# Kernel tuning notes

Measured on AMD Instinct MI355X. Metric: run time of the kernel, lower is better.

Reference implementation:

```python
import jax, jax.numpy as jnp
import numpy as np

N = 50000      # nodes
E = 800000     # edges (before self loops)
D_IN = 64      # input atom feature dim
HID = 128      # hidden_dim
HEADS = 4
C = HID // HEADS  # 32 per-head channels
ED = 12        # edge feature dim
L = 4          # num GAT layers
EPS = 1e-5


def setup_inputs() -> dict:
    key = jax.random.key(0)
    ks = jax.random.split(key, 10)
    s = 0.1
    return {
        "x": jax.random.normal(ks[0], (N, D_IN), jnp.float32),
        "edge_index": jax.random.randint(ks[1], (2, E), 0, N, dtype=jnp.int32),
        "edge_attr": jax.random.uniform(ks[2], (E, ED), jnp.float32),
        "Wp": jax.random.normal(ks[3], (D_IN, HID), jnp.float32) * s,
        "bp": jnp.zeros((HID,), jnp.float32),
        "W": jax.random.normal(ks[4], (L, HID, HID), jnp.float32) * s,
        "We": jax.random.normal(ks[5], (L, ED, HID), jnp.float32) * s,
        "att_src": jax.random.normal(ks[6], (L, HEADS, C), jnp.float32) * s,
        "att_dst": jax.random.normal(ks[7], (L, HEADS, C), jnp.float32) * s,
        "att_edge": jax.random.normal(ks[8], (L, HEADS, C), jnp.float32) * s,
        "bias": jnp.zeros((L, HID), jnp.float32),
        "gamma": jnp.ones((L, HID), jnp.float32),
        "beta": jnp.zeros((L, HID), jnp.float32),
    }


def _gat_layer(h, src, dst, ea_full, W, We, a_s, a_d, a_e, b):
    # PyG GATConv: x' = x W -> [N, heads, C]; attention uses edge features, msg = alpha * x'_src
    xp = (h @ W).reshape(N, HEADS, C)
    e_emb = (ea_full @ We).reshape(-1, HEADS, C)          # [E', heads, C]
    a_src = (xp * a_s).sum(-1)                            # [N, heads]
    a_dst = (xp * a_d).sum(-1)
    a = a_src[src] + a_dst[dst] + (e_emb * a_e).sum(-1)   # [E', heads]
    a = jax.nn.leaky_relu(a, 0.2)
    # segment softmax over destination node neighborhoods
    amax = jax.ops.segment_max(a, dst, num_segments=N)
    ex = jnp.exp(a - amax[dst])
    denom = jax.ops.segment_sum(ex, dst, num_segments=N)
    alpha = ex / denom[dst]                               # [E', heads]
    msg = alpha[:, :, None] * xp[src]                     # [E', heads, C]
    out = jax.ops.segment_sum(msg, dst, num_segments=N)   # [N, heads, C]
    return out.reshape(N, HID) + b


def reference(x, edge_index, edge_attr, Wp, bp, W, We, att_src, att_dst, att_edge, bias, gamma, beta):
    # PyG GATConv add_self_loops=True with fill_value='mean' for edge_attr
    loop = jnp.arange(N, dtype=edge_index.dtype)
    src = jnp.concatenate([edge_index[0], loop])
    dst = jnp.concatenate([edge_index[1], loop])
    ea_mean = edge_attr.mean(0)
    ea_full = jnp.concatenate([edge_attr, jnp.broadcast_to(ea_mean, (N, ED))], 0)

    h = jax.nn.relu(x @ Wp + bp)
    for i in range(L):
        h_in = h
        h = _gat_layer(h, src, dst, ea_full, W[i], We[i], att_src[i], att_dst[i], att_edge[i], bias[i])
        # BatchNorm1d (training-mode batch statistics)
        mu = h.mean(0)
        var = ((h - mu) ** 2).mean(0)
        h = gamma[i] * (h - mu) / jnp.sqrt(var + EPS) + beta[i]
        h = jax.nn.relu(h)
        if i > 0:
            h = h + h_in
    return h
```

## Files before the change

### kernel.cpp

```cpp
#include <hip/hip_runtime.h>

constexpr int N_NODES = 50000;
constexpr int N_EDGES = 800000;
constexpr int N_ETOT  = N_EDGES + N_NODES;
constexpr int HID     = 128;
constexpr int HEADS   = 4;
constexpr int ED      = 12;
constexpr int LAYERS  = 4;
constexpr float BN_EPS = 1e-5f;
constexpr int R_REP = 4;
constexpr int RN = N_NODES * R_REP;
constexpr int SB2 = (RN + 255) / 256;
constexpr int EB = (N_ETOT + 255) / 256;
constexpr int GB = (N_NODES + 63) / 64;
constexpr int WB = (LAYERS * HID * HID + 255) / 256;

typedef __attribute__((ext_vector_type(8))) short short8;
typedef __attribute__((ext_vector_type(4))) float floatx4;

__device__ inline unsigned bf16pair(float a, float b) {
    unsigned ua = __float_as_uint(a), ub = __float_as_uint(b);
    ua = (ua + 0x7FFFu + ((ua >> 16) & 1u)) >> 16;
    ub = (ub + 0x7FFFu + ((ub >> 16) & 1u)) >> 16;
    return ua | (ub << 16);
}

__launch_bounds__(256)
__global__ void pre1_kernel(const int* __restrict__ dst, int* __restrict__ hist2,
                            int* __restrict__ rank,
                            const float* __restrict__ ea, float* __restrict__ easum,
                            const float* __restrict__ W, unsigned short* __restrict__ wb,
                            const float* __restrict__ A, const float* __restrict__ B,
                            const float* __restrict__ bias, float* __restrict__ C,
                            unsigned* __restrict__ Cb) {
    __shared__ float smem[64 * 128];
    int bid = blockIdx.x, t = threadIdx.x;
    if (bid < GB) {
        constexpr int K = 64;
        const float4* B4 = (const float4*)B;
        float4* Bs4 = (float4*)smem;
#pragma unroll
        for (int i = t; i < K * 32; i += 256) Bs4[i] = B4[i];
        __syncthreads();

        int c0 = (t & 15) * 8;
        int r0 = (t >> 4) * 4;
        int rbase = bid * 64 + r0;

        float acc[4][8];
#pragma unroll
        for (int j = 0; j < 4; j++)
#pragma unroll
            for (int c = 0; c < 8; c++) acc[j][c] = 0.f;

        const float4* A4 = (const float4*)A;
        int rg[4];
#pragma unroll
        for (int j = 0; j < 4; j++) rg[j] = min(rbase + j, N_NODES - 1);

        for (int kk = 0; kk < K; kk += 4) {
            float4 av[4];
#pragma unroll
            for (int j = 0; j < 4; j++) av[j] = A4[(size_t)rg[j] * (K / 4) + (kk >> 2)];
            float a_arr[4][4];
#pragma unroll
            for (int j = 0; j < 4; j++) {
                a_arr[j][0] = av[j].x; a_arr[j][1] = av[j].y;
                a_arr[j][2] = av[j].z; a_arr[j][3] = av[j].w;
            }
#pragma unroll
            for (int jj = 0; jj < 4; jj++) {
                float4 b0 = Bs4[(kk + jj) * 32 + (c0 >> 2)];
                float4 b1 = Bs4[(kk + jj) * 32 + (c0 >> 2) + 1];
#pragma unroll
                for (int j = 0; j < 4; j++) {
                    float a = a_arr[j][jj];
                    acc[j][0] += a * b0.x; acc[j][1] += a * b0.y;
                    acc[j][2] += a * b0.z; acc[j][3] += a * b0.w;
                    acc[j][4] += a * b1.x; acc[j][5] += a * b1.y;
                    acc[j][6] += a * b1.z; acc[j][7] += a * b1.w;
                }
            }
        }

#pragma unroll
        for (int j = 0; j < 4; j++) {
            int r = rbase + j;
            if (r < N_NODES) {
                float o[8];
#pragma unroll
                for (int c = 0; c < 8; c++) o[c] = fmaxf(acc[j][c] + bias[c0 + c], 0.f);
                ((float4*)(C + (size_t)r * 128 + c0))[0] = make_float4(o[0], o[1], o[2], o[3]);
                ((float4*)(C + (size_t)r * 128 + c0 + 4))[0] = make_float4(o[4], o[5], o[6], o[7]);
                uint4 pk;
                pk.x = bf16pair(o[0], o[1]); pk.y = bf16pair(o[2], o[3]);
                pk.z = bf16pair(o[4], o[5]); pk.w = bf16pair(o[6], o[7]);
                ((uint4*)(Cb + (size_t)r * 64 + (c0 >> 1)))[0] = pk;
            }
        }
    } else if (bid < GB + EB) {
        int e = (bid - GB) * 256 + t;
        if (e < N_ETOT) {
            int d = (e < N_EDGES) ? dst[e] : (e - N_EDGES);
            rank[e] = atomicAdd(&hist2[(e & (R_REP - 1)) * N_NODES + d], 1);
        }
    } else if (bid < GB + EB + 256) {
        int b2 = bid - GB - EB;
        float* ls = smem;
        if (t < 12) ls[t] = 0.f;
        __syncthreads();
        float loc[12];
#pragma unroll
        for (int d = 0; d < 12; d++) loc[d] = 0.f;
        for (int e = b2 * 256 + t; e < N_EDGES; e += 256 * 256) {
            const float* er = ea + (size_t)e * ED;
#pragma unroll
            for (int d = 0; d < 12; d++) loc[d] += er[d];
        }
#pragma unroll
        for (int d = 0; d < 12; d++) atomicAdd(&ls[d], loc[d]);
        __syncthreads();
        if (t < 12) atomicAdd(&easum[t], ls[t]);
    } else {
        int idx = (bid - GB - EB - 256) * 256 + t;
        if (idx < LAYERS * HID * HID) {
            int l = idx >> 14;
            int k = (idx >> 7) & 127;
            int n = idx & 127;
            unsigned u = __float_as_uint(W[idx]);
            u = (u + 0x7FFFu + ((u >> 16) & 1u)) >> 16;
            int kt = k >> 5, q = (k & 31) >> 3, j = k & 7;
            int nt = n >> 4, c = n & 15;
            int lane = q * 16 + c;
            wb[(size_t)l * 16384 + ((size_t)(kt * 8 + nt) * 64 + lane) * 8 + j] =
                (unsigned short)u;
        }
    }
}

__global__ void blocksum_kernel(const int* __restrict__ hist2, int* __restrict__ bsum) {
    __shared__ int sd[256];
    int t = threadIdx.x;
    int f = blockIdx.x * 256 + t;
    int v = 0;
    if (f < RN) v = hist2[(f & (R_REP - 1)) * N_NODES + (f >> 2)];
    sd[t] = v;
    __syncthreads();
#pragma unroll
    for (int off = 128; off; off >>= 1) {
        if (t < off) sd[t] += sd[t + off];
        __syncthreads();
    }
    if (t == 0) bsum[blockIdx.x] = sd[0];
}

__launch_bounds__(256)
__global__ void pre2_kernel(const int* __restrict__ bsum, int* __restrict__ boff,
                            int* __restrict__ rowpR, const float* __restrict__ easum,
                            const float* __restrict__ We, const float* __restrict__ att_edge,
                            float* __restrict__ wea_all, float* __restrict__ aloop) {
    int t = threadIdx.x;
    if (blockIdx.x == 0) {
        __shared__ int sd[256];
        int b = 4 * t;
        int v0 = (b + 0 < SB2) ? bsum[b + 0] : 0;
        int v1 = (b + 1 < SB2) ? bsum[b + 1] : 0;
        int v2 = (b + 2 < SB2) ? bsum[b + 2] : 0;
        int v3 = (b + 3 < SB2) ? bsum[b + 3] : 0;
        int tot = v0 + v1 + v2 + v3;
        sd[t] = tot;
        __syncthreads();
#pragma unroll
        for (int off = 1; off < 256; off <<= 1) {
            int u = (t >= off) ? sd[t - off] : 0;
            __syncthreads();
            sd[t] += u;
            __syncthreads();
        }
        int excl = sd[t] - tot;
        if (b + 0 < SB2) boff[b + 0] = excl;
        if (b + 1 < SB2) boff[b + 1] = excl + v0;
        if (b + 2 < SB2) boff[b + 2] = excl + v0 + v1;
        if (b + 3 < SB2) boff[b + 3] = excl + v0 + v1 + v2;
        if (t == 255) rowpR[RN] = sd[255];
    } else {
        __shared__ float em[12];
        __shared__ float weash[LAYERS * ED * HEADS];
        if (t < 12) em[t] = easum[t] / (float)N_EDGES;
        if (t < LAYERS * ED * HEADS) {
            int l = t / (ED * HEADS);
            int r = t % (ED * HEADS);
            int d = r / HEADS;
            int h = r % HEADS;
            float sum = 0.f;
#pragma unroll
            for (int c = 0; c < 32; c++)
                sum += We[((size_t)(l * ED + d)) * HID + h * 32 + c] *
                       att_edge[(l * HEADS + h) * 32 + c];
            wea_all[t] = sum;
            weash[t] = sum;
        }
        __syncthreads();
        if (t < LAYERS * HEADS) {
            int l = t / HEADS, h = t % HEADS;
            float s = 0.f;
#pragma unroll
            for (int d = 0; d < 12; d++) s += em[d] * weash[l * ED * HEADS + d * HEADS + h];
            aloop[t] = s;
        }
    }
}

__global__ void rowp_kernel(const int* __restrict__ hist2, const int* __restrict__ boff,
                            int* __restrict__ rowpR) {
    __shared__ int sd[256];
    int t = threadIdx.x;
    int f = blockIdx.x * 256 + t;
    int v = (f < RN) ? hist2[(f & (R_REP - 1)) * N_NODES + (f >> 2)] : 0;
    sd[t] = v;
    __syncthreads();
#pragma unroll
    for (int off = 1; off < 256; off <<= 1) {
        int u = (t >= off) ? sd[t - off] : 0;
        __syncthreads();
        sd[t] += u;
        __syncthreads();
    }
    if (f < RN) rowpR[f] = sd[t] - v + boff[blockIdx.x];
}

__launch_bounds__(256)
__global__ void pre3_kernel(const unsigned short* __restrict__ hAb,
                            const unsigned short* __restrict__ wb,
                            const float* __restrict__ att_s, const float* __restrict__ att_d,
                            unsigned* __restrict__ xpb,
                            float* __restrict__ asrc, float* __restrict__ adst,
                            const int* __restrict__ src, const int* __restrict__ dst,
                            const int* __restrict__ rank, const int* __restrict__ rowpR,
                            int2* __restrict__ csr) {
    __shared__ float smem[4 * 16 * 129];
    int t = threadIdx.x;
    if (blockIdx.x >= GB) {
        int e = (blockIdx.x - GB) * 256 + t;
        if (e >= N_ETOT) return;
        int s, d;
        if (e < N_EDGES) { s = src[e]; d = dst[e]; }
        else             { s = d = e - N_EDGES; }
        int pos = rowpR[d * R_REP + (e & (R_REP - 1))] + rank[e];
        csr[pos] = make_int2(s, e);
        return;
    }
    int bid = blockIdx.x;
    float (*lds)[16][129] = (float (*)[16][129])smem;
    int w = t >> 6, lane = t & 63;
    int rbase = bid * 64 + w * 16;
    int mrow = lane & 15, quad = lane >> 4;

    floatx4 acc[8];
#pragma unroll
    for (int nt = 0; nt < 8; nt++) acc[nt] = (floatx4){0.f, 0.f, 0.f, 0.f};

    int arow = min(rbase + mrow, N_NODES - 1);
    const short8* wb8 = (const short8*)wb;
#pragma unroll
    for (int kt = 0; kt < 4; kt++) {
        short8 afrag = *(const short8*)(hAb + (size_t)arow * 128 + kt * 32 + quad * 8);
#pragma unroll
        for (int nt = 0; nt < 8; nt++) {
            short8 bfrag = wb8[(kt * 8 + nt) * 64 + lane];
            acc[nt] = __builtin_amdgcn_mfma_f32_16x16x32_bf16(afrag, bfrag, acc[nt], 0, 0, 0);
        }
    }
#pragma unroll
    for (int nt = 0; nt < 8; nt++)
#pragma unroll
        for (int rr = 0; rr < 4; rr++)
            lds[w][quad * 4 + rr][nt * 16 + mrow] = acc[nt][rr];

    int row = lane >> 2, h = lane & 3;
    int r = rbase + row;
    float vals[32];
    float ps = 0.f, pd = 0.f;
#pragma unroll
    for (int c = 0; c < 32; c++) {
        float v = lds[w][row][h * 32 + c];
        vals[c] = v;
        ps += v * att_s[h * 32 + c];
        pd += v * att_d[h * 32 + c];
    }
    if (r < N_NODES) {
        unsigned* dstp = xpb + (size_t)r * 64 + h * 16;
#pragma unroll
        for (int qq = 0; qq < 4; qq++) {
            uint4 o;
            o.x = bf16pair(vals[qq * 8 + 0], vals[qq * 8 + 1]);
            o.y = bf16pair(vals[qq * 8 + 2], vals[qq * 8 + 3]);
            o.z = bf16pair(vals[qq * 8 + 4], vals[qq * 8 + 5]);
            o.w = bf16pair(vals[qq * 8 + 6], vals[qq * 8 + 7]);
            ((uint4*)dstp)[qq] = o;
        }
        asrc[r * 4 + h] = ps;
        adst[r * 4 + h] = pd;
    }
}

__launch_bounds__(256)
__global__ void pre4_kernel(const int2* __restrict__ csr, const float* __restrict__ ea,
                            const float* __restrict__ wea_all, const float* __restrict__ aloop,
                            uint2* __restrict__ aecsr) {
    __shared__ float wsh[LAYERS * ED * HEADS];
    __shared__ float lsh[LAYERS * HEADS];
    int t = threadIdx.x;
    if (t < LAYERS * ED * HEADS) wsh[t] = wea_all[t];
    if (t < LAYERS * HEADS) lsh[t] = aloop[t];
    __syncthreads();
    int i = blockIdx.x * 256 + t;
    if (i >= N_ETOT) return;
    int e = csr[i].y;
    float a[LAYERS][4];
    if (e < N_EDGES) {
        float er[12];
        const float* ep = ea + (size_t)e * ED;
#pragma unroll
        for (int d = 0; d < 12; d++) er[d] = ep[d];
#pragma unroll
        for (int l = 0; l < LAYERS; l++)
#pragma unroll
            for (int h = 0; h < 4; h++) {
                float s = 0.f;
#pragma unroll
                for (int d = 0; d < 12; d++) s += er[d] * wsh[l * 48 + d * 4 + h];
                a[l][h] = s;
            }
    } else {
#pragma unroll
        for (int l = 0; l < LAYERS; l++)
#pragma unroll
            for (int h = 0; h < 4; h++) a[l][h] = lsh[l * 4 + h];
    }
#pragma unroll
    for (int l = 0; l < LAYERS; l++)
        aecsr[(size_t)l * N_ETOT + i] =
            make_uint2(bf16pair(a[l][0], a[l][1]), bf16pair(a[l][2], a[l][3]));
}

template <int ADD>
__launch_bounds__(256)
__global__ void gemm_fused_kernel(const float* __restrict__ outb,
                                  const float* __restrict__ bnsum,
                                  const float* __restrict__ bnsum2,
                                  const float* __restrict__ gamma,
                                  const float* __restrict__ beta,
                                  float* __restrict__ hA,
                                  const unsigned short* __restrict__ wb,
                                  const float* __restrict__ att_s,
                                  const float* __restrict__ att_d,
                                  unsigned* __restrict__ xpb,
                                  float* __restrict__ asrc, float* __restrict__ adst) {
    __shared__ float lds[4][16][129];
    __shared__ float sc_s[128], sh_s[128];
    int t = threadIdx.x;
    if (t < 128) {
        float mu = bnsum[t] / (float)N_NODES;
        float var = bnsum2[t] / (float)N_NODES - mu * mu;
        float inv = rsqrtf(var + BN_EPS);
        float g = gamma[t] * inv;
        sc_s[t] = g;
        sh_s[t] = beta[t] - mu * g;
    }
    __syncthreads();

    int w = t >> 6, lane = t & 63;
    int rbase = blockIdx.x * 64 + w * 16;
    int mrow = lane & 15, quad = lane >> 4;
    int arow = rbase + mrow;
    bool owner = arow < N_NODES;
    int ar = min(arow, N_NODES - 1);

    floatx4 acc[8];
#pragma unroll
    for (int nt = 0; nt < 8; nt++) acc[nt] = (floatx4){0.f, 0.f, 0.f, 0.f};

    const short8* wb8 = (const short8*)wb;
#pragma unroll
    for (int kt = 0; kt < 4; kt++) {
        int cb = kt * 32 + quad * 8;
        const float4* ob = (const float4*)(outb + (size_t)ar * 128 + cb);
        float4 o0 = ob[0], o1 = ob[1];
        float v[8];
        v[0] = fmaxf(o0.x * sc_s[cb + 0] + sh_s[cb + 0], 0.f);
        v[1] = fmaxf(o0.y * sc_s[cb + 1] + sh_s[cb + 1], 0.f);
        v[2] = fmaxf(o0.z * sc_s[cb + 2] + sh_s[cb + 2], 0.f);
        v[3] = fmaxf(o0.w * sc_s[cb + 3] + sh_s[cb + 3], 0.f);
        v[4] = fmaxf(o1.x * sc_s[cb + 4] + sh_s[cb + 4], 0.f);
        v[5] = fmaxf(o1.y * sc_s[cb + 5] + sh_s[cb + 5], 0.f);
        v[6] = fmaxf(o1.z * sc_s[cb + 6] + sh_s[cb + 6], 0.f);
        v[7] = fmaxf(o1.w * sc_s[cb + 7] + sh_s[cb + 7], 0.f);
        if (ADD) {
            const float4* hp = (const float4*)(hA + (size_t)ar * 128 + cb);
            float4 h0 = hp[0], h1 = hp[1];
            v[0] += h0.x; v[1] += h0.y; v[2] += h0.z; v[3] += h0.w;
            v[4] += h1.x; v[5] += h1.y; v[6] += h1.z; v[7] += h1.w;
        }
        if (owner) {
            float4* hw = (float4*)(hA + (size_t)ar * 128 + cb);
            hw[0] = make_float4(v[0], v[1], v[2], v[3]);
            hw[1] = make_float4(v[4], v[5], v[6], v[7]);
        }
        uint4 pk;
        pk.x = bf16pair(v[0], v[1]); pk.y = bf16pair(v[2], v[3]);
        pk.z = bf16pair(v[4], v[5]); pk.w = bf16pair(v[6], v[7]);
        short8 afrag = *(short8*)&pk;
#pragma unroll
        for (int nt = 0; nt < 8; nt++) {
            short8 bfrag = wb8[(kt * 8 + nt) * 64 + lane];
            acc[nt] = __builtin_amdgcn_mfma_f32_16x16x32_bf16(afrag, bfrag, acc[nt], 0, 0, 0);
        }
    }

#pragma unroll
    for (int nt = 0; nt < 8; nt++)
#pragma unroll
        for (int rr = 0; rr < 4; rr++)
            lds[w][quad * 4 + rr][nt * 16 + mrow] = acc[nt][rr];

    int row = lane >> 2, h = lane & 3;
    int r = rbase + row;
    float vals[32];
    float ps = 0.f, pd = 0.f;
#pragma unroll
    for (int c = 0; c < 32; c++) {
        float v = lds[w][row][h * 32 + c];
        vals[c] = v;
        ps += v * att_s[h * 32 + c];
        pd += v * att_d[h * 32 + c];
    }
    if (r < N_NODES) {
        unsigned* dstp = xpb + (size_t)r * 64 + h * 16;
#pragma unroll
        for (int qq = 0; qq < 4; qq++) {
            uint4 o;
            o.x = bf16pair(vals[qq * 8 + 0], vals[qq * 8 + 1]);
            o.y = bf16pair(vals[qq * 8 + 2], vals[qq * 8 + 3]);
            o.z = bf16pair(vals[qq * 8 + 4], vals[qq * 8 + 5]);
            o.w = bf16pair(vals[qq * 8 + 6], vals[qq * 8 + 7]);
            ((uint4*)dstp)[qq] = o;
        }
        asrc[r * 4 + h] = ps;
        adst[r * 4 + h] = pd;
    }
}

__launch_bounds__(256)
__global__ void node_kernel(const uint2* __restrict__ aecsr, const float* __restrict__ asrc,
                            const float* __restrict__ adst, const int* __restrict__ rowpR,
                            const int2* __restrict__ csr, const unsigned* __restrict__ xpb,
                            float* __restrict__ out) {
    int gw = (blockIdx.x * blockDim.x + threadIdx.x) >> 6;
    int lane = threadIdx.x & 63;
    if (gw >= N_NODES) return;
    int sub = lane >> 4;
    int sl  = lane & 15;
    int h   = sl >> 2;
    int beg = rowpR[gw * R_REP], end = rowpR[(gw + 1) * R_REP];
    const uint4* xp4 = (const uint4*)xpb;
    float adh = adst[gw * 4 + h];

    float a[8];
#pragma unroll
    for (int c = 0; c < 8; c++) a[c] = 0.f;
    float den = 0.f;

#define PROC(JJ)                                                                 \
    {                                                                            \
        int2 se = csr[JJ];                                                       \
        uint2 ae = aecsr[JJ];                                                    \
        unsigned aw = (h & 2) ? ae.y : ae.x;                                     \
        float aeh = __uint_as_float((h & 1) ? (aw & 0xFFFF0000u) : (aw << 16));  \
        float ash = asrc[se.x * 4 + h];                                          \
        uint4 v = xp4[(size_t)se.x * 16 + sl];                                   \
        float lg = ash + adh + aeh;                                              \
        lg = (lg > 0.f) ? lg : 0.2f * lg;                                        \
        float ex = __expf(fminf(lg, 60.f));                                      \
        a[0] += ex * __uint_as_float(v.x << 16);                                 \
        a[1] += ex * __uint_as_float(v.x & 0xFFFF0000u);                         \
        a[2] += ex * __uint_as_float(v.y << 16);                                 \
        a[3] += ex * __uint_as_float(v.y & 0xFFFF0000u);                         \
        a[4] += ex * __uint_as_float(v.z << 16);                                 \
        a[5] += ex * __uint_as_float(v.z & 0xFFFF0000u);                         \
        a[6] += ex * __uint_as_float(v.w << 16);                                 \
        a[7] += ex * __uint_as_float(v.w & 0xFFFF0000u);                         \
        den += ex;                                                               \
    }

    int j = beg + sub;
    for (; j + 12 < end; j += 16) {
        PROC(j); PROC(j + 4); PROC(j + 8); PROC(j + 12);
    }
    for (; j < end; j += 4) PROC(j);
#undef PROC

#pragma unroll
    for (int c = 0; c < 8; c++) {
        a[c] += __shfl_xor(a[c], 16);
        a[c] += __shfl_xor(a[c], 32);
    }
    den += __shfl_xor(den, 16);
    den += __shfl_xor(den, 32);
    float inv = 1.0f / den;
    if (sub == 0) {
        float* op = out + (size_t)gw * 128 + sl * 8;
        ((float4*)op)[0] = make_float4(a[0] * inv, a[1] * inv, a[2] * inv, a[3] * inv);
        ((float4*)op)[1] = make_float4(a[4] * inv, a[5] * inv, a[6] * inv, a[7] * inv);
    }
}

__launch_bounds__(256)
__global__ void bnstats_kernel(const float* __restrict__ h, float* __restrict__ bnsum,
                               float* __restrict__ bnsum2) {
    __shared__ float ls[256], ls2[256];
    int t = threadIdx.x;
    int c = t & 127, half = t >> 7;
    int r0 = blockIdx.x * 128;
    float s = 0.f, s2 = 0.f;
    int rend = min(r0 + 128, N_NODES);
    for (int r = r0 + half; r < rend; r += 2) {
        float v = h[(size_t)r * 128 + c];
        s += v; s2 += v * v;
    }
    ls[t] = s; ls2[t] = s2;
    __syncthreads();
    if (half == 0) {
        s += ls[t + 128]; s2 += ls2[t + 128];
        atomicAdd(&bnsum[c], s);
        atomicAdd(&bnsum2[c], s2);
    }
}

__launch_bounds__(256)
__global__ void finalupd_kernel(const float* __restrict__ outb, const float* __restrict__ bnsum,
                                const float* __restrict__ bnsum2, const float* __restrict__ gamma,
                                const float* __restrict__ beta, const float* __restrict__ hA,
                                float* __restrict__ dst) {
    __shared__ float sc_s[128], sh_s[128];
    int t = threadIdx.x;
    if (t < 128) {
        float mu = bnsum[t] / (float)N_NODES;
        float var = bnsum2[t] / (float)N_NODES - mu * mu;
        float inv = rsqrtf(var + BN_EPS);
        float g = gamma[t] * inv;
        sc_s[t] = g;
        sh_s[t] = beta[t] - mu * g;
    }
    __syncthreads();
    int i = blockIdx.x * blockDim.x + t;
    if (i >= N_NODES * 32) return;
    int c4 = (i & 31) * 4;
    float4 o = ((const float4*)outb)[i];
    float4 hh = ((const float4*)hA)[i];
    float4 v;
    v.x = fmaxf(o.x * sc_s[c4 + 0] + sh_s[c4 + 0], 0.f) + hh.x;
    v.y = fmaxf(o.y * sc_s[c4 + 1] + sh_s[c4 + 1], 0.f) + hh.y;
    v.z = fmaxf(o.z * sc_s[c4 + 2] + sh_s[c4 + 2], 0.f) + hh.z;
    v.w = fmaxf(o.w * sc_s[c4 + 3] + sh_s[c4 + 3], 0.f) + hh.w;
    ((float4*)dst)[i] = v;
}

extern "C" void kernel_launch(void* const* d_in, const int* in_sizes, int n_in,
                              void* d_out, int out_size, void* d_ws, size_t ws_size,
                              hipStream_t stream) {
    const float* x          = (const float*)d_in[0];
    const int*   edge_index = (const int*)d_in[1];
    const float* edge_attr  = (const float*)d_in[2];
    const float* Wp         = (const float*)d_in[3];
    const float* bp         = (const float*)d_in[4];
    const float* W          = (const float*)d_in[5];
    const float* We         = (const float*)d_in[6];
    const float* att_src    = (const float*)d_in[7];
    const float* att_dst    = (const float*)d_in[8];
    const float* att_edge   = (const float*)d_in[9];
    const float* gamma      = (const float*)d_in[11];
    const float* beta       = (const float*)d_in[12];
    float* outp = (float*)d_out;

    const int* ei_src = edge_index;
    const int* ei_dst = edge_index + N_EDGES;

    char* p = (char*)d_ws;
    auto alloc = [&](size_t nbytes) {
        char* r = p;
        p += (nbytes + 255) & ~(size_t)255;
        return r;
    };
    int*   hist2    = (int*)alloc((size_t)RN * 4);
    float* easum    = (float*)alloc(16 * 4);
    float* bnsumall = (float*)alloc((size_t)LAYERS * 256 * 4);
    size_t zero_bytes = (char*)(bnsumall + LAYERS * 256) - (char*)hist2;

    float* hA       = (float*)alloc((size_t)N_NODES * 128 * 4);
    unsigned* hAb   = (unsigned*)alloc((size_t)N_NODES * 64 * 4);
    unsigned* xpb   = (unsigned*)alloc((size_t)N_NODES * 64 * 4);
    float* outb     = (float*)alloc((size_t)N_NODES * 128 * 4);
    float* asrc     = (float*)alloc((size_t)N_NODES * 4 * 4);
    float* adst     = (float*)alloc((size_t)N_NODES * 4 * 4);
    float* wea_all  = (float*)alloc((LAYERS * 48 + 16) * 4);
    float* aloop    = wea_all + LAYERS * 48;
    unsigned short* wb = (unsigned short*)alloc((size_t)LAYERS * 16384 * 2);
    int* rowpR      = (int*)alloc(((size_t)RN + 1) * 4);
    int* rankbuf    = (int*)alloc((size_t)N_ETOT * 4);
    int2* csr       = (int2*)alloc((size_t)N_ETOT * 8);
    uint2* aecsr    = (uint2*)alloc((size_t)LAYERS * N_ETOT * 8);
    int* bsum       = (int*)alloc(1024 * 4);
    int* boff       = (int*)alloc(1024 * 4);

    (void)hipMemsetAsync(hist2, 0, zero_bytes, stream);

    pre1_kernel<<<GB + EB + 256 + WB, 256, 0, stream>>>(
        ei_dst, hist2, rankbuf, edge_attr, easum, W, wb, x, Wp, bp, hA, hAb);
    blocksum_kernel<<<SB2, 256, 0, stream>>>(hist2, bsum);
    pre2_kernel<<<2, 256, 0, stream>>>(bsum, boff, rowpR, easum, We, att_edge, wea_all, aloop);
    rowp_kernel<<<SB2, 256, 0, stream>>>(hist2, boff, rowpR);
    pre3_kernel<<<GB + EB, 256, 0, stream>>>(
        (const unsigned short*)hAb, wb, att_src, att_dst, xpb, asrc, adst,
        ei_src, ei_dst, rankbuf, rowpR, csr);
    pre4_kernel<<<EB, 256, 0, stream>>>(csr, edge_attr, wea_all, aloop, aecsr);

    for (int l = 0; l < LAYERS; l++) {
        float* bnsum  = bnsumall + l * 256;
        float* bnsum2 = bnsum + 128;
        node_kernel<<<(N_NODES + 3) / 4, 256, 0, stream>>>(
            aecsr + (size_t)l * N_ETOT, asrc, adst, rowpR, csr, xpb, outb);
        bnstats_kernel<<<(N_NODES + 127) / 128, 256, 0, stream>>>(outb, bnsum, bnsum2);
        if (l < LAYERS - 1) {
            if (l == 0)
                gemm_fused_kernel<0><<<GB, 256, 0, stream>>>(
                    outb, bnsum, bnsum2, gamma + l * 128, beta + l * 128, hA,
                    wb + (size_t)(l + 1) * 16384, att_src + (l + 1) * 128,
                    att_dst + (l + 1) * 128, xpb, asrc, adst);
            else
                gemm_fused_kernel<1><<<GB, 256, 0, stream>>>(
                    outb, bnsum, bnsum2, gamma + l * 128, beta + l * 128, hA,
                    wb + (size_t)(l + 1) * 16384, att_src + (l + 1) * 128,
                    att_dst + (l + 1) * 128, xpb, asrc, adst);
        } else {
            finalupd_kernel<<<(N_NODES * 32 + 255) / 256, 256, 0, stream>>>(
                outb, bnsum, bnsum2, gamma + l * 128, beta + l * 128, hA, outp);
        }
    }
}
```

Before: 597.5 us.

## Build CSR via two-level chunked bucket sort instead of global atomic ranking

Replaces the per-edge global-atomic histogram and rank approach (with 4x replicated counters) with a two-pass bucketed sort. Edges are first counted per 128-node bucket per 2048-edge chunk in shared memory, then prefix-scanned and scattered into bucket order. A new per-bucket kernel then sorts edges by local destination in shared memory to produce the CSR and rowp. This cuts contention from global atomics and the random writes they cause, at the cost of an extra bucketed buffer, an extra kernel and a second pass over the edges. Edge order within a node is now set by shared-memory atomics, so it is nondeterministic and float summation order may vary between runs.

New measurement: 569.5 us. 4.7% less time.

```diff
diff --git a/kernel.cpp b/kernel.cpp
--- a/kernel.cpp
+++ b/kernel.cpp
@@ -8,12 +8,14 @@
 constexpr int ED      = 12;
 constexpr int LAYERS  = 4;
 constexpr float BN_EPS = 1e-5f;
-constexpr int R_REP = 4;
-constexpr int RN = N_NODES * R_REP;
-constexpr int SB2 = (RN + 255) / 256;
 constexpr int EB = (N_ETOT + 255) / 256;
 constexpr int GB = (N_NODES + 63) / 64;
 constexpr int WB = (LAYERS * HID * HID + 255) / 256;
+constexpr int CHUNK  = 2048;
+constexpr int NCHUNK = (N_ETOT + CHUNK - 1) / CHUNK;
+constexpr int NB     = (N_NODES + 127) / 128;
+constexpr int F_TOT  = NB * NCHUNK;
+constexpr int SB3    = (F_TOT + 255) / 256;
 
 typedef __attribute__((ext_vector_type(8))) short short8;
 typedef __attribute__((ext_vector_type(4))) float floatx4;
@@ -26,8 +28,7 @@
 }
 
 __launch_bounds__(256)
-__global__ void pre1_kernel(const int* __restrict__ dst, int* __restrict__ hist2,
-                            int* __restrict__ rank,
+__global__ void pre1_kernel(const int* __restrict__ dst, int* __restrict__ counts,
                             const float* __restrict__ ea, float* __restrict__ easum,
                             const float* __restrict__ W, unsigned short* __restrict__ wb,
                             const float* __restrict__ A, const float* __restrict__ B,
@@ -98,14 +99,21 @@
                 ((uint4*)(Cb + (size_t)r * 64 + (c0 >> 1)))[0] = pk;
             }
         }
-    } else if (bid < GB + EB) {
-        int e = (bid - GB) * 256 + t;
-        if (e < N_ETOT) {
+    } else if (bid < GB + NCHUNK) {
+        int chunk = bid - GB;
+        int* lh = (int*)smem;
+        for (int i = t; i < NB; i += 256) lh[i] = 0;
+        __syncthreads();
+        int e0 = chunk * CHUNK;
+        int eend = min(e0 + CHUNK, N_ETOT);
+        for (int e = e0 + t; e < eend; e += 256) {
             int d = (e < N_EDGES) ? dst[e] : (e - N_EDGES);
-            rank[e] = atomicAdd(&hist2[(e & (R_REP - 1)) * N_NODES + d], 1);
-        }
-    } else if (bid < GB + EB + 256) {
-        int b2 = bid - GB - EB;
+            atomicAdd(&lh[d >> 7], 1);
+        }
+        __syncthreads();
+        for (int i = t; i < NB; i += 256) counts[(size_t)chunk * NB + i] = lh[i];
+    } else if (bid < GB + NCHUNK + 256) {
+        int b2 = bid - GB - NCHUNK;
         float* ls = smem;
         if (t < 12) ls[t] = 0.f;
         __syncthreads();
@@ -122,7 +130,7 @@
         __syncthreads();
         if (t < 12) atomicAdd(&easum[t], ls[t]);
     } else {
-        int idx = (bid - GB - EB - 256) * 256 + t;
+        int idx = (bid - GB - NCHUNK - 256) * 256 + t;
         if (idx < LAYERS * HID * HID) {
             int l = idx >> 14;
             int k = (idx >> 7) & 127;
@@ -138,12 +146,15 @@
     }
 }
 
-__global__ void blocksum_kernel(const int* __restrict__ hist2, int* __restrict__ bsum) {
+__global__ void blocksum2_kernel(const int* __restrict__ counts, int* __restrict__ bsum) {
     __shared__ int sd[256];
     int t = threadIdx.x;
-    int f = blockIdx.x * 256 + t;
+    int j = blockIdx.x * 256 + t;
     int v = 0;
-    if (f < RN) v = hist2[(f & (R_REP - 1)) * N_NODES + (f >> 2)];
+    if (j < F_TOT) {
+        int bb = j / NCHUNK, cc = j - bb * NCHUNK;
+        v = counts[(size_t)cc * NB + bb];
+    }
     sd[t] = v;
     __syncthreads();
 #pragma unroll
@@ -156,18 +167,18 @@
 
 __launch_bounds__(256)
 __global__ void pre2_kernel(const int* __restrict__ bsum, int* __restrict__ boff,
-                            int* __restrict__ rowpR, const float* __restrict__ easum,
+                            int* __restrict__ chunkbase, int* __restrict__ rowp,
+                            const float* __restrict__ easum,
                             const float* __restrict__ We, const float* __restrict__ att_edge,
                             float* __restrict__ wea_all, float* __restrict__ aloop) {
     int t = threadIdx.x;
     if (blockIdx.x == 0) {
         __shared__ int sd[256];
-        int b = 4 * t;
-        int v0 = (b + 0 < SB2) ? bsum[b + 0] : 0;
-        int v1 = (b + 1 < SB2) ? bsum[b + 1] : 0;
-        int v2 = (b + 2 < SB2) ? bsum[b + 2] : 0;
-        int v3 = (b + 3 < SB2) ? bsum[b + 3] : 0;
-        int tot = v0 + v1 + v2 + v3;
+        int b = 3 * t;
+        int v0 = (b + 0 < SB3) ? bsum[b + 0] : 0;
+        int v1 = (b + 1 < SB3) ? bsum[b + 1] : 0;
+        int v2 = (b + 2 < SB3) ? bsum[b + 2] : 0;
+        int tot = v0 + v1 + v2;
         sd[t] = tot;
         __syncthreads();
 #pragma unroll
@@ -178,11 +189,13 @@
             __syncthreads();
         }
         int excl = sd[t] - tot;
-        if (b + 0 < SB2) boff[b + 0] = excl;
-        if (b + 1 < SB2) boff[b + 1] = excl + v0;
-        if (b + 2 < SB2) boff[b + 2] = excl + v0 + v1;
-        if (b + 3 < SB2) boff[b + 3] = excl + v0 + v1 + v2;
-        if (t == 255) rowpR[RN] = sd[255];
+        if (b + 0 < SB3) boff[b + 0] = excl;
+        if (b + 1 < SB3) boff[b + 1] = excl + v0;
+        if (b + 2 < SB3) boff[b + 2] = excl + v0 + v1;
+        if (t == 255) {
+            chunkbase[F_TOT] = sd[255];
+            rowp[N_NODES] = N_ETOT;
+        }
     } else {
         __shared__ float em[12];
         __shared__ float weash[LAYERS * ED * HEADS];
@@ -211,12 +224,16 @@
     }
 }
 
-__global__ void rowp_kernel(const int* __restrict__ hist2, const int* __restrict__ boff,
-                            int* __restrict__ rowpR) {
+__global__ void addback_kernel(const int* __restrict__ counts, const int* __restrict__ boff,
+                               int* __restrict__ chunkbase) {
     __shared__ int sd[256];
     int t = threadIdx.x;
-    int f = blockIdx.x * 256 + t;
-    int v = (f < RN) ? hist2[(f & (R_REP - 1)) * N_NODES + (f >> 2)] : 0;
+    int j = blockIdx.x * 256 + t;
+    int v = 0;
+    if (j < F_TOT) {
+        int bb = j / NCHUNK, cc = j - bb * NCHUNK;
+        v = counts[(size_t)cc * NB + bb];
+    }
     sd[t] = v;
     __syncthreads();
 #pragma unroll
@@ -226,7 +243,7 @@
         sd[t] += u;
         __syncthreads();
     }
-    if (f < RN) rowpR[f] = sd[t] - v + boff[blockIdx.x];
+    if (j < F_TOT) chunkbase[j] = sd[t] - v + boff[blockIdx.x];
 }
 
 __launch_bounds__(256)
@@ -236,18 +253,28 @@
                             unsigned* __restrict__ xpb,
                             float* __restrict__ asrc, float* __restrict__ adst,
                             const int* __restrict__ src, const int* __restrict__ dst,
-                            const int* __restrict__ rank, const int* __restrict__ rowpR,
-                            int2* __restrict__ csr) {
+                            const int* __restrict__ chunkbase, int2* __restrict__ bucketed) {
     __shared__ float smem[4 * 16 * 129];
     int t = threadIdx.x;
     if (blockIdx.x >= GB) {
-        int e = (blockIdx.x - GB) * 256 + t;
-        if (e >= N_ETOT) return;
-        int s, d;
-        if (e < N_EDGES) { s = src[e]; d = dst[e]; }
-        else             { s = d = e - N_EDGES; }
-        int pos = rowpR[d * R_REP + (e & (R_REP - 1))] + rank[e];
-        csr[pos] = make_int2(s, e);
+        int chunk = blockIdx.x - GB;
+        int* lb = (int*)smem;
+        int* lh = lb + NB;
+        for (int i = t; i < NB; i += 256) {
+            lb[i] = chunkbase[(size_t)i * NCHUNK + chunk];
+            lh[i] = 0;
+        }
+        __syncthreads();
+        int e0 = chunk * CHUNK;
+        int eend = min(e0 + CHUNK, N_ETOT);
+        for (int e = e0 + t; e < eend; e += 256) {
+            int s, d;
+            if (e < N_EDGES) { s = src[e]; d = dst[e]; }
+            else             { s = d = e - N_EDGES; }
+            int b = d >> 7;
+            int lr = atomicAdd(&lh[b], 1);
+            bucketed[lb[b] + lr] = make_int2(s, e | ((d & 127) << 20));
+        }
         return;
     }
     int bid = blockIdx.x;
@@ -301,6 +328,42 @@
         }
         asrc[r * 4 + h] = ps;
         adst[r * 4 + h] = pd;
+    }
+}
+
+__launch_bounds__(256)
+__global__ void csrd_kernel(const int2* __restrict__ bucketed, const int* __restrict__ chunkbase,
+                            int2* __restrict__ csr, int* __restrict__ rowp) {
+    __shared__ int hist[128], exc[128], cur[128];
+    int b = blockIdx.x, t = threadIdx.x;
+    int base = chunkbase[(size_t)b * NCHUNK];
+    int cend = chunkbase[(size_t)(b + 1) * NCHUNK];
+    int cnt = cend - base;
+    if (t < 128) { hist[t] = 0; cur[t] = 0; }
+    __syncthreads();
+    for (int i = t; i < cnt; i += 256)
+        atomicAdd(&hist[(bucketed[base + i].y >> 20) & 127], 1);
+    __syncthreads();
+    if (t < 128) exc[t] = hist[t];
+    __syncthreads();
+#pragma unroll
+    for (int off = 1; off < 128; off <<= 1) {
+        int u = (t < 128 && t >= off) ? exc[t - off] : 0;
+        __syncthreads();
+        if (t < 128) exc[t] += u;
+        __syncthreads();
+    }
+    if (t < 128) {
+        exc[t] -= hist[t];
+        int node = b * 128 + t;
+        if (node < N_NODES) rowp[node] = base + exc[t];
+    }
+    __syncthreads();
+    for (int i = t; i < cnt; i += 256) {
+        int2 r = bucketed[base + i];
+        int dl = (r.y >> 20) & 127;
+        int lr = atomicAdd(&cur[dl], 1);
+        csr[base + exc[dl] + lr] = make_int2(r.x, r.y & 0xFFFFF);
     }
 }
 
@@ -453,7 +516,7 @@
 
 __launch_bounds__(256)
 __global__ void node_kernel(const uint2* __restrict__ aecsr, const float* __restrict__ asrc,
-                            const float* __restrict__ adst, const int* __restrict__ rowpR,
+                            const float* __restrict__ adst, const int* __restrict__ rowp,
                             const int2* __restrict__ csr, const unsigned* __restrict__ xpb,
                             float* __restrict__ out) {
     int gw = (blockIdx.x * blockDim.x + threadIdx.x) >> 6;
@@ -462,7 +525,7 @@
     int sub = lane >> 4;
     int sl  = lane & 15;
     int h   = sl >> 2;
-    int beg = rowpR[gw * R_REP], end = rowpR[(gw + 1) * R_REP];
+    int beg = rowp[gw], end = rowp[gw + 1];
     const uint4* xp4 = (const uint4*)xpb;
     float adh = adst[gw * 4 + h];
 
@@ -592,10 +655,9 @@
         p += (nbytes + 255) & ~(size_t)255;
         return r;
     };
-    int*   hist2    = (int*)alloc((size_t)RN * 4);
     float* easum    = (float*)alloc(16 * 4);
     float* bnsumall = (float*)alloc((size_t)LAYERS * 256 * 4);
-    size_t zero_bytes = (char*)(bnsumall + LAYERS * 256) - (char*)hist2;
+    size_t zero_bytes = (char*)(bnsumall + LAYERS * 256) - (char*)easum;
 
     float* hA       = (float*)alloc((size_t)N_NODES * 128 * 4);
     unsigned* hAb   = (unsigned*)alloc((size_t)N_NODES * 64 * 4);
@@ -606,30 +668,34 @@
     float* wea_all  = (float*)alloc((LAYERS * 48 + 16) * 4);
     float* aloop    = wea_all + LAYERS * 48;
     unsigned short* wb = (unsigned short*)alloc((size_t)LAYERS * 16384 * 2);
-    int* rowpR      = (int*)alloc(((size_t)RN + 1) * 4);
-    int* rankbuf    = (int*)alloc((size_t)N_ETOT * 4);
+    int* rowp       = (int*)alloc(((size_t)N_NODES + 1) * 4);
+    int* counts     = (int*)alloc((size_t)F_TOT * 4);
+    int* chunkbase  = (int*)alloc(((size_t)F_TOT + 1) * 4);
+    int2* bucketed  = (int2*)alloc((size_t)N_ETOT * 8);
     int2* csr       = (int2*)alloc((size_t)N_ETOT * 8);
     uint2* aecsr    = (uint2*)alloc((size_t)LAYERS * N_ETOT * 8);
     int* bsum       = (int*)alloc(1024 * 4);
     int* boff       = (int*)alloc(1024 * 4);
 
-    (void)hipMemsetAsync(hist2, 0, zero_bytes, stream);
-
-    pre1_kernel<<<GB + EB + 256 + WB, 256, 0, stream>>>(
-        ei_dst, hist2, rankbuf, edge_attr, easum, W, wb, x, Wp, bp, hA, hAb);
-    blocksum_kernel<<<SB2, 256, 0, stream>>>(hist2, bsum);
-    pre2_kernel<<<2, 256, 0, stream>>>(bsum, boff, rowpR, easum, We, att_edge, wea_all, aloop);
-    rowp_kernel<<<SB2, 256, 0, stream>>>(hist2, boff, rowpR);
-    pre3_kernel<<<GB + EB, 256, 0, stream>>>(
+    (void)hipMemsetAsync(easum, 0, zero_bytes, stream);
+
+    pre1_kernel<<<GB + NCHUNK + 256 + WB, 256, 0, stream>>>(
+        ei_dst, counts, edge_attr, easum, W, wb, x, Wp, bp, hA, hAb);
+    blocksum2_kernel<<<SB3, 256, 0, stream>>>(counts, bsum);
+    pre2_kernel<<<2, 256, 0, stream>>>(bsum, boff, chunkbase, rowp, easum, We, att_edge,
+                                       wea_all, aloop);
+    addback_kernel<<<SB3, 256, 0, stream>>>(counts, boff, chunkbase);
+    pre3_kernel<<<GB + NCHUNK, 256, 0, stream>>>(
         (const unsigned short*)hAb, wb, att_src, att_dst, xpb, asrc, adst,
-        ei_src, ei_dst, rankbuf, rowpR, csr);
+        ei_src, ei_dst, chunkbase, bucketed);
+    csrd_kernel<<<NB, 256, 0, stream>>>(bucketed, chunkbase, csr, rowp);
     pre4_kernel<<<EB, 256, 0, stream>>>(csr, edge_attr, wea_all, aloop, aecsr);
 
     for (int l = 0; l < LAYERS; l++) {
         float* bnsum  = bnsumall + l * 256;
         float* bnsum2 = bnsum + 128;
         node_kernel<<<(N_NODES + 3) / 4, 256, 0, stream>>>(
-            aecsr + (size_t)l * N_ETOT, asrc, adst, rowpR, csr, xpb, outb);
+            aecsr + (size_t)l * N_ETOT, asrc, adst, rowp, csr, xpb, outb);
         bnstats_kernel<<<(N_NODES + 127) / 128, 256, 0, stream>>>(outb, bnsum, bnsum2);
         if (l < LAYERS - 1) {
             if (l == 0)
```
